# Performance work log

Measured on AMD Instinct MI355X. Metric: run time of the kernel, lower is better.

Reference implementation:

```python
import jax, jax.numpy as jnp
import numpy as np

B, S, E, H = 32, 4096, 1024, 16
D = E // H  # head_dim = 64


def setup_inputs() -> dict:
    key = jax.random.key(0)
    ks = jax.random.split(key, 6)
    scale = 1.0 / np.sqrt(E)
    x = jax.random.normal(ks[0], (B, S, E), dtype=jnp.float32)
    mask = jax.random.randint(ks[1], (B, S), 0, 2).astype(bool)  # True = masked key
    in_proj_w = jax.random.uniform(ks[2], (3 * E, E), jnp.float32, -scale, scale)
    in_proj_b = jnp.zeros((3 * E,), jnp.float32)
    out_w = jax.random.uniform(ks[3], (E, E), jnp.float32, -scale, scale)
    out_b = jnp.zeros((E,), jnp.float32)
    return {"x": x, "mask": mask, "in_proj_w": in_proj_w, "in_proj_b": in_proj_b,
            "out_w": out_w, "out_b": out_b}


def reference(x, mask, in_proj_w, in_proj_b, out_w, out_b):
    # nn.MultiheadAttention with q = x[:, 0:1, :], k = v = x, key_padding_mask=mask
    Wq, Wk, Wv = in_proj_w[:E], in_proj_w[E:2 * E], in_proj_w[2 * E:]
    bq, bk, bv = in_proj_b[:E], in_proj_b[E:2 * E], in_proj_b[2 * E:]
    q = (x[:, 0, :] @ Wq.T + bq).reshape(B, H, D)            # (B,H,D)
    k = (x @ Wk.T + bk).reshape(B, S, H, D)                  # (B,S,H,D)
    v = (x @ Wv.T + bv).reshape(B, S, H, D)
    scores = jnp.einsum('bhd,bshd->bhs', q, k) / np.sqrt(D)  # (B,H,S)
    scores = jnp.where(mask[:, None, :], jnp.float32(-1e30), scores)
    attn = jax.nn.softmax(scores, axis=-1)                   # (B,H,S)
    ctx = jnp.einsum('bhs,bshd->bhd', attn, v).reshape(B, E)
    out = ctx @ out_w.T + out_b                              # (B,E) == attn_output.squeeze(1)
    attn_weights = attn.mean(axis=1)[:, None, :]             # (B,1,S): heads averaged
    return out, attn_weights
```

## Files before the change

### kernel.cpp

```cpp
#include <hip/hip_runtime.h>
#include <math.h>


constexpr int cB = 32, cS = 4096, cE = 1024, cH = 16, cD = 64, cNC = 16;

constexpr size_t OFF_P    = 0;
constexpr size_t OFF_C    = OFF_P + 524288;
constexpr size_t OFF_Q    = OFF_C + 512;
constexpr size_t OFF_SC   = OFF_Q + 32768;
constexpr size_t OFF_SM   = OFF_SC + 2097152;
constexpr size_t OFF_SL   = OFF_SM + 8192;
constexpr size_t OFF_MF   = OFF_SL + 8192;
constexpr size_t OFF_IL   = OFF_MF + 512;
constexpr size_t OFF_CTX  = OFF_IL + 512;
constexpr size_t OFF_PART = OFF_CTX + 32768;
constexpr size_t OFF_Y    = OFF_PART + 8388608;

__device__ inline float wave_max64(float v) {
#pragma unroll
  for (int m = 1; m < 64; m <<= 1) v = fmaxf(v, __shfl_xor(v, m));
  return v;
}
__device__ inline float wave_sum64(float v) {
#pragma unroll
  for (int m = 1; m < 64; m <<= 1) v += __shfl_xor(v, m);
  return v;
}

__global__ __launch_bounds__(256) void kgemm32(const float* __restrict__ A,
                                               size_t aRowStride, int aBlk,
                                               const float* __restrict__ Wm, int wRow0,
                                               const float* __restrict__ bias,
                                               float* __restrict__ C) {
  __shared__ float a_lds[32 * 1028];
  __shared__ float red[4][16][32];
  int tid = threadIdx.x;
  int bx = blockIdx.x;
  const float* abase = A + (aBlk ? ((size_t)(bx >> 2) * 1024) : (size_t)0);

#pragma unroll 4
  for (int j = 0; j < 32; ++j) {
    float4 v = *(const float4*)(abase + (size_t)j * aRowStride + (size_t)tid * 4);
    *(float4*)(a_lds + j * 1028 + tid * 4) = v;
  }
  __syncthreads();

  int wv = tid >> 6, lane = tid & 63;
  int ng = lane >> 4, bp = lane & 15;
  float acc[4][2];
#pragma unroll
  for (int j = 0; j < 4; ++j) { acc[j][0] = 0.f; acc[j][1] = 0.f; }

  const float* w0 = Wm + (size_t)(wRow0 + bx * 16 + ng * 4) * 1024;
#pragma unroll 4
  for (int i = 0; i < 64; ++i) {
    int e4 = wv * 64 + ((i + bp) & 63);
    float4 a0 = *(const float4*)(a_lds + (bp * 2 + 0) * 1028 + e4 * 4);
    float4 a1 = *(const float4*)(a_lds + (bp * 2 + 1) * 1028 + e4 * 4);
#pragma unroll
    for (int j = 0; j < 4; ++j) {
      float4 w4 = *(const float4*)(w0 + (size_t)j * 1024 + e4 * 4);
      acc[j][0] = fmaf(w4.x, a0.x, acc[j][0]); acc[j][0] = fmaf(w4.y, a0.y, acc[j][0]);
      acc[j][0] = fmaf(w4.z, a0.z, acc[j][0]); acc[j][0] = fmaf(w4.w, a0.w, acc[j][0]);
      acc[j][1] = fmaf(w4.x, a1.x, acc[j][1]); acc[j][1] = fmaf(w4.y, a1.y, acc[j][1]);
      acc[j][1] = fmaf(w4.z, a1.z, acc[j][1]); acc[j][1] = fmaf(w4.w, a1.w, acc[j][1]);
    }
  }
#pragma unroll
  for (int j = 0; j < 4; ++j) {
    red[wv][ng * 4 + j][bp * 2 + 0] = acc[j][0];
    red[wv][ng * 4 + j][bp * 2 + 1] = acc[j][1];
  }
  __syncthreads();
#pragma unroll
  for (int t = 0; t < 2; ++t) {
    int idx = t * 256 + tid;
    int n = idx >> 5, b = idx & 31;
    float s = red[0][n][b] + red[1][n][b] + red[2][n][b] + red[3][n][b] +
              bias[bx * 16 + n];
    C[(size_t)b * 1024 + bx * 16 + n] = s;
  }
}

__global__ __launch_bounds__(256) void kp_gemm(const float* __restrict__ w,
                                               const float* __restrict__ bvec,
                                               const float* __restrict__ q,
                                               float* __restrict__ p,
                                               float* __restrict__ cb) {
  __shared__ float w_lds[64 * 260];
  __shared__ float q_lds[32 * 65];
  int h = blockIdx.x >> 2, et = blockIdx.x & 3;
  int tid = threadIdx.x;
#pragma unroll 4
  for (int j = 0; j < 16; ++j) {
    int idx = j * 256 + tid;
    int row = idx >> 6, c4 = idx & 63;
    float4 v = *(const float4*)(w + (size_t)(1024 + h * 64 + row) * 1024 + et * 256 + c4 * 4);
    *(float4*)(w_lds + row * 260 + c4 * 4) = v;
  }
#pragma unroll
  for (int jj = 0; jj < 2; ++jj) {
    int idx = jj * 256 + tid;
    int row = idx >> 4, c4 = idx & 15;
    float4 v = *(const float4*)(q + (size_t)row * 1024 + h * 64 + c4 * 4);
    *(float4*)(q_lds + row * 65 + c4 * 4) = v;
  }
  __syncthreads();

  int b = tid & 31, eg = tid >> 5;
  float4 acc[8];
#pragma unroll
  for (int j = 0; j < 8; ++j) acc[j] = make_float4(0.f, 0.f, 0.f, 0.f);
#pragma unroll 4
  for (int d = 0; d < 64; ++d) {
    float qv = q_lds[b * 65 + d];
#pragma unroll
    for (int j = 0; j < 8; ++j) {
      float4 wv4 = *(const float4*)(w_lds + d * 260 + eg * 32 + j * 4);
      acc[j].x = fmaf(wv4.x, qv, acc[j].x);
      acc[j].y = fmaf(wv4.y, qv, acc[j].y);
      acc[j].z = fmaf(wv4.z, qv, acc[j].z);
      acc[j].w = fmaf(wv4.w, qv, acc[j].w);
    }
  }
  float* pb = p + (size_t)(b * cH + h) * cE + et * 256 + eg * 32;
#pragma unroll
  for (int j = 0; j < 8; ++j) {
    float4 o = make_float4(acc[j].x * 0.125f, acc[j].y * 0.125f,
                           acc[j].z * 0.125f, acc[j].w * 0.125f);
    *(float4*)(pb + j * 4) = o;
  }
  if (et == 0 && tid < 32) {
    int bb = tid;
    float cacc = 0.f;
    for (int d = 0; d < 64; ++d)
      cacc = fmaf(q_lds[bb * 65 + d], bvec[1024 + h * 64 + d], cacc);
    cb[bb * cH + h] = 0.125f * cacc;
  }
}

__global__ __launch_bounds__(256) void kfuse2(const float* __restrict__ x,
                                              const float* __restrict__ p,
                                              const float* __restrict__ cbias,
                                              const int* __restrict__ mask,
                                              float* __restrict__ scores,
                                              float* __restrict__ statsM,
                                              float* __restrict__ statsL,
                                              float* __restrict__ part) {
  __shared__ __align__(16) float smem[16384];
  __shared__ float sml_m[4][8], sml_l[4][8];
  int bx = blockIdx.x;
  int b = bx >> 4, sc = bx & 15;
  int s_base = sc * 256;
  int tid = threadIdx.x;
  int wv = tid >> 6, lane = tid & 63;
  int sg = wv & 1, hg = wv >> 1;
  int h0 = __builtin_amdgcn_readfirstlane(hg * 8);
  float acc[2][8];
#pragma unroll
  for (int i = 0; i < 2; ++i)
#pragma unroll
    for (int j = 0; j < 8; ++j) acc[i][j] = 0.f;

  const float* xb = x + ((size_t)b * cS + s_base) * cE;
  const float* __restrict__ pu = p + (size_t)(b * cH + h0) * cE;

  float4 sv[8];
  int r_ = tid >> 3, c4_ = tid & 7;

#pragma unroll
  for (int i = 0; i < 8; ++i)
    sv[i] = *(const float4*)(xb + (size_t)(i * 32 + r_) * cE + c4_ * 4);
  {
    float* xd = smem;
#pragma unroll
    for (int i = 0; i < 8; ++i) {
      int r = i * 32 + r_;
      float vv[4] = {sv[i].x, sv[i].y, sv[i].z, sv[i].w};
#pragma unroll
      for (int j = 0; j < 4; ++j) {
        int e = c4_ * 4 + j;
        int f = (e ^ (e >> 4)) & 15;
        xd[e * 256 + ((((r >> 2) ^ f) << 2) | (r & 3))] = vv[j];
      }
    }
  }
  __syncthreads();

  int gbase = sg * 32 + (lane >> 1);
  int goff = (lane & 1) << 1;
  for (int kt = 1; kt <= 32; ++kt) {
    if (kt < 32) {
#pragma unroll
      for (int i = 0; i < 8; ++i)
        sv[i] = *(const float4*)(xb + (size_t)(i * 32 + r_) * cE + kt * 32 + c4_ * 4);
    }
    {
      const float* xs = smem + ((kt - 1) & 1) * 8192;
      const int kb = (kt - 1) * 32;
#pragma unroll 8
      for (int e = 0; e < 32; ++e) {
        int f = (e ^ (e >> 4)) & 15;
        float2 xv = *(const float2*)&xs[e * 256 + (((gbase ^ f) << 2) | goff)];
        float p0 = pu[kb + e];
        float p1 = pu[cE + kb + e];
        float p2 = pu[2 * cE + kb + e];
        float p3 = pu[3 * cE + kb + e];
        float p4 = pu[4 * cE + kb + e];
        float p5 = pu[5 * cE + kb + e];
        float p6 = pu[6 * cE + kb + e];
        float p7 = pu[7 * cE + kb + e];
        float pa[8] = {p0, p1, p2, p3, p4, p5, p6, p7};
#pragma unroll
        for (int hj = 0; hj < 8; ++hj) {
          acc[0][hj] = fmaf(xv.x, pa[hj], acc[0][hj]);
          acc[1][hj] = fmaf(xv.y, pa[hj], acc[1][hj]);
        }
      }
    }
    if (kt < 32) {
      float* xd = smem + (kt & 1) * 8192;
#pragma unroll
      for (int i = 0; i < 8; ++i) {
        int r = i * 32 + r_;
        float vv[4] = {sv[i].x, sv[i].y, sv[i].z, sv[i].w};
#pragma unroll
        for (int j = 0; j < 4; ++j) {
          int e = c4_ * 4 + j;
          int f = (e ^ (e >> 4)) & 15;
          xd[e * 256 + ((((r >> 2) ^ f) << 2) | (r & 3))] = vv[j];
        }
      }
    }
    __syncthreads();
  }

  float* al = smem;
  int sl_loc = sg * 128 + lane * 2;
  int sl = s_base + sl_loc;
  float ca[8];
  {
    float4 c0 = *(const float4*)(cbias + b * cH + h0);
    float4 c1 = *(const float4*)(cbias + b * cH + h0 + 4);
    ca[0] = c0.x; ca[1] = c0.y; ca[2] = c0.z; ca[3] = c0.w;
    ca[4] = c1.x; ca[5] = c1.y; ca[6] = c1.z; ca[7] = c1.w;
  }
  int2 mv = *(const int2*)(mask + (size_t)b * cS + sl);
  float vs0[8], vs1[8];
#pragma unroll
  for (int hj = 0; hj < 8; ++hj) {
    float v0 = mv.x ? -1e30f : acc[0][hj] + ca[hj];
    float v1 = mv.y ? -1e30f : acc[1][hj] + ca[hj];
    vs0[hj] = v0; vs1[hj] = v1;
    float2 o = make_float2(v0, v1);
    *(float2*)(scores + (size_t)(b * cH + h0 + hj) * cS + sl) = o;
    float wm = wave_max64(fmaxf(v0, v1));
    if (lane == 0) sml_m[wv][hj] = wm;
  }
  __syncthreads();
#pragma unroll
  for (int hj = 0; hj < 8; ++hj) {
    float mh = fmaxf(sml_m[hg * 2][hj], sml_m[hg * 2 + 1][hj]);
    float e0 = __expf(vs0[hj] - mh);
    float e1 = __expf(vs1[hj] - mh);
    float ws = wave_sum64(e0 + e1);
    if (lane == 0) sml_l[wv][hj] = ws;
    al[(sl_loc + 0) * 20 + h0 + hj] = e0;
    al[(sl_loc + 1) * 20 + h0 + hj] = e1;
  }
  __syncthreads();
  if (tid < 16) {
    int h = tid, hg2 = h >> 3, hj = h & 7;
    float mh = fmaxf(sml_m[hg2 * 2][hj], sml_m[hg2 * 2 + 1][hj]);
    float L = sml_l[hg2 * 2][hj] + sml_l[hg2 * 2 + 1][hj];
    statsM[(size_t)(b * cH + h) * cNC + sc] = mh;
    statsL[(size_t)(b * cH + h) * cNC + sc] = L;
  }

  float4 acc2[16];
#pragma unroll
  for (int h = 0; h < cH; ++h) acc2[h] = make_float4(0.f, 0.f, 0.f, 0.f);
  const float* xg = xb + (size_t)tid * 4;
#pragma unroll 4
  for (int s = 255; s >= 0; --s) {
    float4 xv = *(const float4*)(xg + (size_t)s * cE);
    const float4* ar = (const float4*)(al + s * 20);
    float4 a0 = ar[0], a1 = ar[1], a2 = ar[2], a3 = ar[3];
    float aa[16] = {a0.x, a0.y, a0.z, a0.w, a1.x, a1.y, a1.z, a1.w,
                    a2.x, a2.y, a2.z, a2.w, a3.x, a3.y, a3.z, a3.w};
#pragma unroll
    for (int h = 0; h < cH; ++h) {
      acc2[h].x = fmaf(aa[h], xv.x, acc2[h].x);
      acc2[h].y = fmaf(aa[h], xv.y, acc2[h].y);
      acc2[h].z = fmaf(aa[h], xv.z, acc2[h].z);
      acc2[h].w = fmaf(aa[h], xv.w, acc2[h].w);
    }
  }
  float* pb = part + ((size_t)(b * cNC + sc) * cH) * cE + (size_t)tid * 4;
#pragma unroll
  for (int h = 0; h < cH; ++h) *(float4*)(pb + (size_t)h * cE) = acc2[h];
}

__global__ __launch_bounds__(256) void k5a_comb(const float* __restrict__ part,
                                                const float* __restrict__ statsM,
                                                const float* __restrict__ statsL,
                                                float* __restrict__ y,
                                                float* __restrict__ Mf,
                                                float* __restrict__ iLf) {
  int b = blockIdx.x >> 4, h = blockIdx.x & 15;
  int bh = b * cH + h;
  int tid = threadIdx.x;
  float M = -3e38f;
#pragma unroll
  for (int c = 0; c < cNC; ++c) M = fmaxf(M, statsM[bh * cNC + c]);
  float L = 0.f;
  float wgt[cNC];
#pragma unroll
  for (int c = 0; c < cNC; ++c) {
    wgt[c] = __expf(statsM[bh * cNC + c] - M);
    L += statsL[bh * cNC + c] * wgt[c];
  }
  float iL = 1.0f / L;
  if (tid == 0) { Mf[bh] = M; iLf[bh] = iL; }
  float4 a = make_float4(0.f, 0.f, 0.f, 0.f);
  const float* pb = part + (size_t)b * cNC * cH * cE + (size_t)h * cE + (size_t)tid * 4;
#pragma unroll
  for (int c = 0; c < cNC; ++c) {
    float4 v = *(const float4*)(pb + (size_t)c * cH * cE);
    a.x = fmaf(v.x, wgt[c], a.x); a.y = fmaf(v.y, wgt[c], a.y);
    a.z = fmaf(v.z, wgt[c], a.z); a.w = fmaf(v.w, wgt[c], a.w);
  }
  a.x *= iL; a.y *= iL; a.z *= iL; a.w *= iL;
  *(float4*)(y + (size_t)bh * cE + (size_t)tid * 4) = a;
}

__global__ __launch_bounds__(256) void kmean(const float* __restrict__ scores,
                                             const float* __restrict__ Mf,
                                             const float* __restrict__ iLf,
                                             float* __restrict__ out) {
  int idx = blockIdx.x * 256 + threadIdx.x;
  int b = idx >> 12, s = idx & 4095;
  float sum = 0.f;
#pragma unroll
  for (int h = 0; h < cH; ++h) {
    float v = scores[(size_t)(b * cH + h) * cS + s];
    sum += __expf(v - Mf[b * cH + h]) * iLf[b * cH + h];
  }
  out[cB * cE + (size_t)b * cS + s] = sum * (1.0f / 16.0f);
}

extern "C" void kernel_launch(void* const* d_in, const int* in_sizes, int n_in,
                              void* d_out, int out_size, void* d_ws, size_t ws_size,
                              hipStream_t stream) {
  const float* x = (const float*)d_in[0];
  const int* mask = (const int*)d_in[1];
  const float* in_proj_w = (const float*)d_in[2];
  const float* in_proj_b = (const float*)d_in[3];
  const float* out_w = (const float*)d_in[4];
  const float* out_b = (const float*)d_in[5];
  float* out = (float*)d_out;
  float* W = (float*)d_ws;

  float* p = W + OFF_P;
  float* cb = W + OFF_C;
  float* q = W + OFF_Q;
  float* scores = W + OFF_SC;
  float* statsM = W + OFF_SM;
  float* statsL = W + OFF_SL;
  float* Mf = W + OFF_MF;
  float* iLf = W + OFF_IL;
  float* ctx = W + OFF_CTX;
  float* part = W + OFF_PART;
  float* y = W + OFF_Y;

  kgemm32<<<64, 256, 0, stream>>>(x, (size_t)cS * cE, 0, in_proj_w, 0, in_proj_b, q);
  kp_gemm<<<64, 256, 0, stream>>>(in_proj_w, in_proj_b, q, p, cb);
  kfuse2<<<512, 256, 0, stream>>>(x, p, cb, mask, scores, statsM, statsL, part);
  k5a_comb<<<512, 256, 0, stream>>>(part, statsM, statsL, y, Mf, iLf);
  kgemm32<<<64, 256, 0, stream>>>(y, (size_t)cH * cE, 1, in_proj_w, 2048,
                                  in_proj_b + 2048, ctx);
  kmean<<<512, 256, 0, stream>>>(scores, Mf, iLf, out);
  kgemm32<<<64, 256, 0, stream>>>(ctx, (size_t)cE, 0, out_w, 0, out_b, out);
}
```

Measured before the change: 300.7 us.

## Restructure fused score kernel into streaming online-softmax over row tiles

The main fused kernel used to make two passes over each 256-row chunk of x: one to compute the scores and one to re-read x from global memory for the weighted sum. It now streams 16-row tiles of full 1024-wide x rows into LDS, computes scores with cross-lane shuffle reductions, and updates a running max and sum (online softmax). The weighted accumulation reuses the same LDS tile, so x is read from HBM only once per block. The cost is a 64KB LDS tile, several more barriers per tile, rescaling of 64 accumulator registers per tile and higher register pressure, which may lower occupancy.

```diff
diff --git a/kernel.cpp b/kernel.cpp
--- a/kernel.cpp
+++ b/kernel.cpp
@@ -16,15 +16,13 @@
 constexpr size_t OFF_PART = OFF_CTX + 32768;
 constexpr size_t OFF_Y    = OFF_PART + 8388608;
 
-__device__ inline float wave_max64(float v) {
-#pragma unroll
-  for (int m = 1; m < 64; m <<= 1) v = fmaxf(v, __shfl_xor(v, m));
-  return v;
-}
 __device__ inline float wave_sum64(float v) {
 #pragma unroll
   for (int m = 1; m < 64; m <<= 1) v += __shfl_xor(v, m);
   return v;
+}
+__device__ inline float sel4(float a0, float a1, float a2, float a3, int i) {
+  return i == 0 ? a0 : (i == 1 ? a1 : (i == 2 ? a2 : a3));
 }
 
 __global__ __launch_bounds__(256) void kgemm32(const float* __restrict__ A,
@@ -37,20 +35,17 @@
   int tid = threadIdx.x;
   int bx = blockIdx.x;
   const float* abase = A + (aBlk ? ((size_t)(bx >> 2) * 1024) : (size_t)0);
-
 #pragma unroll 4
   for (int j = 0; j < 32; ++j) {
     float4 v = *(const float4*)(abase + (size_t)j * aRowStride + (size_t)tid * 4);
     *(float4*)(a_lds + j * 1028 + tid * 4) = v;
   }
   __syncthreads();
-
   int wv = tid >> 6, lane = tid & 63;
   int ng = lane >> 4, bp = lane & 15;
   float acc[4][2];
 #pragma unroll
   for (int j = 0; j < 4; ++j) { acc[j][0] = 0.f; acc[j][1] = 0.f; }
-
   const float* w0 = Wm + (size_t)(wRow0 + bx * 16 + ng * 4) * 1024;
 #pragma unroll 4
   for (int i = 0; i < 64; ++i) {
@@ -106,7 +101,6 @@
     *(float4*)(q_lds + row * 65 + c4 * 4) = v;
   }
   __syncthreads();
-
   int b = tid & 31, eg = tid >> 5;
   float4 acc[8];
 #pragma unroll
@@ -139,166 +133,193 @@
   }
 }
 
-__global__ __launch_bounds__(256) void kfuse2(const float* __restrict__ x,
+__global__ __launch_bounds__(256) void kfuse3(const float* __restrict__ x,
                                               const float* __restrict__ p,
-                                              const float* __restrict__ cbias,
+                                              const float* __restrict__ cbv,
                                               const int* __restrict__ mask,
                                               float* __restrict__ scores,
                                               float* __restrict__ statsM,
                                               float* __restrict__ statsL,
                                               float* __restrict__ part) {
-  __shared__ __align__(16) float smem[16384];
-  __shared__ float sml_m[4][8], sml_l[4][8];
+  __shared__ __align__(16) float xt[16 * 1024];
+  __shared__ __align__(16) float exl[16][20];
+  __shared__ float smax[4][16], ssum[4][16], scl[16];
   int bx = blockIdx.x;
   int b = bx >> 4, sc = bx & 15;
-  int s_base = sc * 256;
+  int s0g = sc * 256;
   int tid = threadIdx.x;
-  int wv = tid >> 6, lane = tid & 63;
-  int sg = wv & 1, hg = wv >> 1;
-  int h0 = __builtin_amdgcn_readfirstlane(hg * 8);
-  float acc[2][8];
-#pragma unroll
-  for (int i = 0; i < 2; ++i)
-#pragma unroll
-    for (int j = 0; j < 8; ++j) acc[i][j] = 0.f;
-
-  const float* xb = x + ((size_t)b * cS + s_base) * cE;
-  const float* __restrict__ pu = p + (size_t)(b * cH + h0) * cE;
-
-  float4 sv[8];
-  int r_ = tid >> 3, c4_ = tid & 7;
-
-#pragma unroll
-  for (int i = 0; i < 8; ++i)
-    sv[i] = *(const float4*)(xb + (size_t)(i * 32 + r_) * cE + c4_ * 4);
+  int sq = tid >> 6;
+  int l = tid & 63;
+  int hg = l >> 4, eg = l & 15;
+  int egx = eg & 7;
+  int st_s = tid >> 4, st_q = tid & 15;
+  int sigB = (tid & ~15) | ((tid & 15) ^ ((tid >> 4) & 7));
+
+  const float* xrow = x + ((size_t)b * cS + s0g) * cE;
+  const float* pbase = p + (size_t)(b * cH + hg * 4) * cE;
+
+  float4 rv[16];
   {
-    float* xd = smem;
-#pragma unroll
-    for (int i = 0; i < 8; ++i) {
-      int r = i * 32 + r_;
-      float vv[4] = {sv[i].x, sv[i].y, sv[i].z, sv[i].w};
-#pragma unroll
-      for (int j = 0; j < 4; ++j) {
-        int e = c4_ * 4 + j;
-        int f = (e ^ (e >> 4)) & 15;
-        xd[e * 256 + ((((r >> 2) ^ f) << 2) | (r & 3))] = vv[j];
+    const float* src = xrow + (size_t)st_s * cE + st_q * 64;
+#pragma unroll
+    for (int i = 0; i < 16; ++i) rv[i] = *(const float4*)(src + i * 4);
+  }
+  float m_run[4], l_run[4];
+#pragma unroll
+  for (int j = 0; j < 4; ++j) { m_run[j] = -3e38f; l_run[j] = 0.f; }
+  float4 acc2[16];
+#pragma unroll
+  for (int h = 0; h < 16; ++h) acc2[h] = make_float4(0.f, 0.f, 0.f, 0.f);
+  float4 cbl = *(const float4*)(cbv + b * cH + hg * 4);
+  float cba[4] = {cbl.x, cbl.y, cbl.z, cbl.w};
+
+#pragma unroll 1
+  for (int t = 0; t < 16; ++t) {
+#pragma unroll
+    for (int i = 0; i < 16; ++i) {
+      int stidx = st_s * 256 + st_q * 16 + (i ^ (st_q & 7));
+      *(float4*)(xt + stidx * 4) = rv[i];
+    }
+    if (t < 15) {
+      const float* src = xrow + (size_t)((t + 1) * 16 + st_s) * cE + st_q * 64;
+#pragma unroll
+      for (int i = 0; i < 16; ++i) rv[i] = *(const float4*)(src + i * 4);
+    }
+    __syncthreads();
+
+    float acc[4][4];
+#pragma unroll
+    for (int s = 0; s < 4; ++s)
+#pragma unroll
+      for (int h = 0; h < 4; ++h) acc[s][h] = 0.f;
+#pragma unroll
+    for (int k = 0; k < 16; ++k) {
+      int col = eg * 16 + (k ^ egx);
+      float4 xv0 = *(const float4*)(xt + ((sq * 4 + 0) * 256 + col) * 4);
+      float4 xv1 = *(const float4*)(xt + ((sq * 4 + 1) * 256 + col) * 4);
+      float4 xv2 = *(const float4*)(xt + ((sq * 4 + 2) * 256 + col) * 4);
+      float4 xv3 = *(const float4*)(xt + ((sq * 4 + 3) * 256 + col) * 4);
+      float4 pv0 = *(const float4*)(pbase + 0 * cE + eg * 64 + k * 4);
+      float4 pv1 = *(const float4*)(pbase + 1 * cE + eg * 64 + k * 4);
+      float4 pv2 = *(const float4*)(pbase + 2 * cE + eg * 64 + k * 4);
+      float4 pv3 = *(const float4*)(pbase + 3 * cE + eg * 64 + k * 4);
+      float4 xa[4] = {xv0, xv1, xv2, xv3};
+      float4 pa[4] = {pv0, pv1, pv2, pv3};
+#pragma unroll
+      for (int s = 0; s < 4; ++s)
+#pragma unroll
+        for (int h = 0; h < 4; ++h) {
+          acc[s][h] = fmaf(xa[s].x, pa[h].x, acc[s][h]);
+          acc[s][h] = fmaf(xa[s].y, pa[h].y, acc[s][h]);
+          acc[s][h] = fmaf(xa[s].z, pa[h].z, acc[s][h]);
+          acc[s][h] = fmaf(xa[s].w, pa[h].w, acc[s][h]);
+        }
+    }
+#pragma unroll
+    for (int m = 1; m < 16; m <<= 1)
+#pragma unroll
+      for (int s = 0; s < 4; ++s)
+#pragma unroll
+        for (int h = 0; h < 4; ++h) acc[s][h] += __shfl_xor(acc[s][h], m);
+#pragma unroll
+    for (int s = 0; s < 4; ++s)
+#pragma unroll
+      for (int h = 0; h < 4; ++h) acc[s][h] += cba[h];
+    {
+      int4 mv = *(const int4*)(mask + (size_t)b * cS + s0g + t * 16 + sq * 4);
+      if (mv.x) { acc[0][0] = -1e30f; acc[0][1] = -1e30f; acc[0][2] = -1e30f; acc[0][3] = -1e30f; }
+      if (mv.y) { acc[1][0] = -1e30f; acc[1][1] = -1e30f; acc[1][2] = -1e30f; acc[1][3] = -1e30f; }
+      if (mv.z) { acc[2][0] = -1e30f; acc[2][1] = -1e30f; acc[2][2] = -1e30f; acc[2][3] = -1e30f; }
+      if (mv.w) { acc[3][0] = -1e30f; acc[3][1] = -1e30f; acc[3][2] = -1e30f; acc[3][3] = -1e30f; }
+    }
+    float tm[4];
+#pragma unroll
+    for (int h = 0; h < 4; ++h)
+      tm[h] = fmaxf(fmaxf(acc[0][h], acc[1][h]), fmaxf(acc[2][h], acc[3][h]));
+    int hsel = eg >> 2, ssel = eg & 3;
+    if (ssel == 0) smax[sq][hg * 4 + hsel] = sel4(tm[0], tm[1], tm[2], tm[3], hsel);
+    __syncthreads();
+    float mnew[4], rs[4];
+#pragma unroll
+    for (int h = 0; h < 4; ++h) {
+      int H = hg * 4 + h;
+      float wm = fmaxf(fmaxf(smax[0][H], smax[1][H]), fmaxf(smax[2][H], smax[3][H]));
+      mnew[h] = fmaxf(m_run[h], wm);
+      rs[h] = __expf(m_run[h] - mnew[h]);
+    }
+    float exv[4][4], psum[4];
+#pragma unroll
+    for (int h = 0; h < 4; ++h) {
+      psum[h] = 0.f;
+#pragma unroll
+      for (int s = 0; s < 4; ++s) {
+        exv[s][h] = __expf(acc[s][h] - mnew[h]);
+        psum[h] += exv[s][h];
       }
     }
-  }
-  __syncthreads();
-
-  int gbase = sg * 32 + (lane >> 1);
-  int goff = (lane & 1) << 1;
-  for (int kt = 1; kt <= 32; ++kt) {
-    if (kt < 32) {
-#pragma unroll
-      for (int i = 0; i < 8; ++i)
-        sv[i] = *(const float4*)(xb + (size_t)(i * 32 + r_) * cE + kt * 32 + c4_ * 4);
-    }
     {
-      const float* xs = smem + ((kt - 1) & 1) * 8192;
-      const int kb = (kt - 1) * 32;
-#pragma unroll 8
-      for (int e = 0; e < 32; ++e) {
-        int f = (e ^ (e >> 4)) & 15;
-        float2 xv = *(const float2*)&xs[e * 256 + (((gbase ^ f) << 2) | goff)];
-        float p0 = pu[kb + e];
-        float p1 = pu[cE + kb + e];
-        float p2 = pu[2 * cE + kb + e];
-        float p3 = pu[3 * cE + kb + e];
-        float p4 = pu[4 * cE + kb + e];
-        float p5 = pu[5 * cE + kb + e];
-        float p6 = pu[6 * cE + kb + e];
-        float p7 = pu[7 * cE + kb + e];
-        float pa[8] = {p0, p1, p2, p3, p4, p5, p6, p7};
-#pragma unroll
-        for (int hj = 0; hj < 8; ++hj) {
-          acc[0][hj] = fmaf(xv.x, pa[hj], acc[0][hj]);
-          acc[1][hj] = fmaf(xv.y, pa[hj], acc[1][hj]);
-        }
+      float r0 = sel4(acc[0][0], acc[0][1], acc[0][2], acc[0][3], hsel);
+      float r1 = sel4(acc[1][0], acc[1][1], acc[1][2], acc[1][3], hsel);
+      float r2 = sel4(acc[2][0], acc[2][1], acc[2][2], acc[2][3], hsel);
+      float r3 = sel4(acc[3][0], acc[3][1], acc[3][2], acc[3][3], hsel);
+      float myscore = sel4(r0, r1, r2, r3, ssel);
+      float e0 = sel4(exv[0][0], exv[0][1], exv[0][2], exv[0][3], hsel);
+      float e1 = sel4(exv[1][0], exv[1][1], exv[1][2], exv[1][3], hsel);
+      float e2 = sel4(exv[2][0], exv[2][1], exv[2][2], exv[2][3], hsel);
+      float e3 = sel4(exv[3][0], exv[3][1], exv[3][2], exv[3][3], hsel);
+      float myex = sel4(e0, e1, e2, e3, ssel);
+      scores[(size_t)(b * cH + hg * 4 + hsel) * cS + s0g + t * 16 + sq * 4 + ssel] = myscore;
+      exl[sq * 4 + ssel][hg * 4 + hsel] = myex;
+    }
+    if (ssel == 0) {
+      ssum[sq][hg * 4 + hsel] = sel4(psum[0], psum[1], psum[2], psum[3], hsel);
+      if (sq == 0) scl[hg * 4 + hsel] = sel4(rs[0], rs[1], rs[2], rs[3], hsel);
+    }
+    __syncthreads();
+#pragma unroll
+    for (int h = 0; h < 4; ++h) {
+      int H = hg * 4 + h;
+      float ts = ssum[0][H] + ssum[1][H] + ssum[2][H] + ssum[3][H];
+      l_run[h] = l_run[h] * rs[h] + ts;
+      m_run[h] = mnew[h];
+    }
+    {
+      const float4* sc4 = (const float4*)scl;
+      float4 s0 = sc4[0], s1 = sc4[1], s2 = sc4[2], s3 = sc4[3];
+      float sca[16] = {s0.x, s0.y, s0.z, s0.w, s1.x, s1.y, s1.z, s1.w,
+                       s2.x, s2.y, s2.z, s2.w, s3.x, s3.y, s3.z, s3.w};
+#pragma unroll
+      for (int h = 0; h < 16; ++h) {
+        acc2[h].x *= sca[h]; acc2[h].y *= sca[h];
+        acc2[h].z *= sca[h]; acc2[h].w *= sca[h];
       }
     }
-    if (kt < 32) {
-      float* xd = smem + (kt & 1) * 8192;
-#pragma unroll
-      for (int i = 0; i < 8; ++i) {
-        int r = i * 32 + r_;
-        float vv[4] = {sv[i].x, sv[i].y, sv[i].z, sv[i].w};
-#pragma unroll
-        for (int j = 0; j < 4; ++j) {
-          int e = c4_ * 4 + j;
-          int f = (e ^ (e >> 4)) & 15;
-          xd[e * 256 + ((((r >> 2) ^ f) << 2) | (r & 3))] = vv[j];
-        }
+#pragma unroll
+    for (int s = 0; s < 16; ++s) {
+      float4 xv = *(const float4*)(xt + (s * 256 + sigB) * 4);
+      const float4* er = (const float4*)(&exl[s][0]);
+      float4 e0 = er[0], e1 = er[1], e2 = er[2], e3 = er[3];
+      float ea[16] = {e0.x, e0.y, e0.z, e0.w, e1.x, e1.y, e1.z, e1.w,
+                      e2.x, e2.y, e2.z, e2.w, e3.x, e3.y, e3.z, e3.w};
+#pragma unroll
+      for (int h = 0; h < 16; ++h) {
+        acc2[h].x = fmaf(ea[h], xv.x, acc2[h].x);
+        acc2[h].y = fmaf(ea[h], xv.y, acc2[h].y);
+        acc2[h].z = fmaf(ea[h], xv.z, acc2[h].z);
+        acc2[h].w = fmaf(ea[h], xv.w, acc2[h].w);
       }
     }
     __syncthreads();
   }
 
-  float* al = smem;
-  int sl_loc = sg * 128 + lane * 2;
-  int sl = s_base + sl_loc;
-  float ca[8];
-  {
-    float4 c0 = *(const float4*)(cbias + b * cH + h0);
-    float4 c1 = *(const float4*)(cbias + b * cH + h0 + 4);
-    ca[0] = c0.x; ca[1] = c0.y; ca[2] = c0.z; ca[3] = c0.w;
-    ca[4] = c1.x; ca[5] = c1.y; ca[6] = c1.z; ca[7] = c1.w;
-  }
-  int2 mv = *(const int2*)(mask + (size_t)b * cS + sl);
-  float vs0[8], vs1[8];
-#pragma unroll
-  for (int hj = 0; hj < 8; ++hj) {
-    float v0 = mv.x ? -1e30f : acc[0][hj] + ca[hj];
-    float v1 = mv.y ? -1e30f : acc[1][hj] + ca[hj];
-    vs0[hj] = v0; vs1[hj] = v1;
-    float2 o = make_float2(v0, v1);
-    *(float2*)(scores + (size_t)(b * cH + h0 + hj) * cS + sl) = o;
-    float wm = wave_max64(fmaxf(v0, v1));
-    if (lane == 0) sml_m[wv][hj] = wm;
-  }
-  __syncthreads();
-#pragma unroll
-  for (int hj = 0; hj < 8; ++hj) {
-    float mh = fmaxf(sml_m[hg * 2][hj], sml_m[hg * 2 + 1][hj]);
-    float e0 = __expf(vs0[hj] - mh);
-    float e1 = __expf(vs1[hj] - mh);
-    float ws = wave_sum64(e0 + e1);
-    if (lane == 0) sml_l[wv][hj] = ws;
-    al[(sl_loc + 0) * 20 + h0 + hj] = e0;
-    al[(sl_loc + 1) * 20 + h0 + hj] = e1;
-  }
-  __syncthreads();
-  if (tid < 16) {
-    int h = tid, hg2 = h >> 3, hj = h & 7;
-    float mh = fmaxf(sml_m[hg2 * 2][hj], sml_m[hg2 * 2 + 1][hj]);
-    float L = sml_l[hg2 * 2][hj] + sml_l[hg2 * 2 + 1][hj];
-    statsM[(size_t)(b * cH + h) * cNC + sc] = mh;
-    statsL[(size_t)(b * cH + h) * cNC + sc] = L;
-  }
-
-  float4 acc2[16];
-#pragma unroll
-  for (int h = 0; h < cH; ++h) acc2[h] = make_float4(0.f, 0.f, 0.f, 0.f);
-  const float* xg = xb + (size_t)tid * 4;
-#pragma unroll 4
-  for (int s = 255; s >= 0; --s) {
-    float4 xv = *(const float4*)(xg + (size_t)s * cE);
-    const float4* ar = (const float4*)(al + s * 20);
-    float4 a0 = ar[0], a1 = ar[1], a2 = ar[2], a3 = ar[3];
-    float aa[16] = {a0.x, a0.y, a0.z, a0.w, a1.x, a1.y, a1.z, a1.w,
-                    a2.x, a2.y, a2.z, a2.w, a3.x, a3.y, a3.z, a3.w};
-#pragma unroll
-    for (int h = 0; h < cH; ++h) {
-      acc2[h].x = fmaf(aa[h], xv.x, acc2[h].x);
-      acc2[h].y = fmaf(aa[h], xv.y, acc2[h].y);
-      acc2[h].z = fmaf(aa[h], xv.z, acc2[h].z);
-      acc2[h].w = fmaf(aa[h], xv.w, acc2[h].w);
-    }
+  if (sq == 0 && (eg & 3) == 0) {
+    int H = hg * 4 + (eg >> 2);
+    statsM[(size_t)(b * cH + H) * cNC + sc] = sel4(m_run[0], m_run[1], m_run[2], m_run[3], eg >> 2);
+    statsL[(size_t)(b * cH + H) * cNC + sc] = sel4(l_run[0], l_run[1], l_run[2], l_run[3], eg >> 2);
   }
   float* pb = part + ((size_t)(b * cNC + sc) * cH) * cE + (size_t)tid * 4;
 #pragma unroll
-  for (int h = 0; h < cH; ++h) *(float4*)(pb + (size_t)h * cE) = acc2[h];
+  for (int h = 0; h < 16; ++h) *(float4*)(pb + (size_t)h * cE) = acc2[h];
 }
 
 __global__ __launch_bounds__(256) void k5a_comb(const float* __restrict__ part,
@@ -375,7 +396,7 @@
 
   kgemm32<<<64, 256, 0, stream>>>(x, (size_t)cS * cE, 0, in_proj_w, 0, in_proj_b, q);
   kp_gemm<<<64, 256, 0, stream>>>(in_proj_w, in_proj_b, q, p, cb);
-  kfuse2<<<512, 256, 0, stream>>>(x, p, cb, mask, scores, statsM, statsL, part);
+  kfuse3<<<512, 256, 0, stream>>>(x, p, cb, mask, scores, statsM, statsL, part);
   k5a_comb<<<512, 256, 0, stream>>>(part, statsM, statsL, y, Mf, iLf);
   kgemm32<<<64, 256, 0, stream>>>(y, (size_t)cH * cE, 1, in_proj_w, 2048,
                                   in_proj_b + 2048, ctx);
```

Measured after the change: 605.7 us. 2.01x slower.
